# Performance work log

Hardware: AMD Instinct MI355X
Metric: run time of the kernel (lower is better)

## Reference

```python
import math
import jax, jax.numpy as jnp
import numpy as np

B, S, D_MODEL = 2, 4096, 1024
N_HEADS, D_KV = 16, 64
INNER = N_HEADS * D_KV
BLOCK_LEN = 128          # local_radius(127) + 1
GLOBAL_BLOCK = 16
NUM_BUCKETS, MAX_DIST = 32, 128
EPS = 1e-6
NEG = -1e10


def _rel_bucket(rp):
    # T5 bidirectional relative position bucketing
    nb = NUM_BUCKETS // 2
    buckets = jnp.where(rp > 0, nb, 0).astype(jnp.int32)
    rp = jnp.abs(rp)
    max_exact = nb // 2
    is_small = rp < max_exact
    rp_f = jnp.maximum(rp, 1).astype(jnp.float32)
    rp_large = max_exact + (jnp.log(rp_f / max_exact) / math.log(MAX_DIST / max_exact) * (nb - max_exact)).astype(jnp.int32)
    rp_large = jnp.minimum(rp_large, nb - 1)
    return buckets + jnp.where(is_small, rp.astype(jnp.int32), rp_large)


def _concat3(x, block_dim, seq_dim):
    # concatenate [prev, self, next] blocks along seq_dim (zero-padded at edges)
    nblk = x.shape[block_dim]
    pad = [(0, 0)] * x.ndim
    pad[block_dim] = (1, 1)
    xp = jnp.pad(x, pad)
    blocks = [jax.lax.slice_in_dim(xp, i, i + nblk, axis=block_dim) for i in range(3)]
    return jnp.concatenate(blocks, axis=seq_dim)


def _global_block_ids(mask):
    # faithful port of _make_global_fixed_block_ids
    b, s = mask.shape
    fixed = jnp.cumsum(jnp.full_like(mask, 1.0 / GLOBAL_BLOCK), axis=1) - 1.0 / GLOBAL_BLOCK
    m = jnp.where(mask != 0.0, 1.0, -1000.0).astype(mask.dtype)
    gids = jnp.floor(m + fixed - 1.0)
    gids = jnp.maximum(gids, -1.0)
    gids = gids * mask + (mask - 1.0)
    block_ends = (jnp.arange(s) % GLOBAL_BLOCK) == GLOBAL_BLOCK - 1
    true_ends = jnp.logical_and(block_ends[None, :], gids >= 0)
    full_blocks = true_ends.sum(-1, keepdims=True).astype(gids.dtype) - 1.0
    gids = jnp.where(gids < full_blocks, gids, full_blocks)
    ng = s // GLOBAL_BLOCK
    seq_max = jnp.max(gids, axis=-1, keepdims=True)
    gseg = jnp.where(jnp.arange(ng)[None, :] <= seq_max, 1, 0)
    return gids.astype(jnp.int32), gseg.astype(jnp.int32)


def setup_inputs() -> dict:
    key = jax.random.key(0)
    ks = jax.random.split(key, 8)
    sc = D_MODEL ** -0.5
    return {
        "hidden_states": jax.random.normal(ks[0], (B, S, D_MODEL), jnp.float32),
        "mask": jnp.ones((B, S), jnp.float32),
        "Wq": jax.random.normal(ks[1], (D_MODEL, INNER), jnp.float32) * sc,
        "Wk": jax.random.normal(ks[2], (D_MODEL, INNER), jnp.float32) * sc,
        "Wv": jax.random.normal(ks[3], (D_MODEL, INNER), jnp.float32) * sc,
        "Wo": jax.random.normal(ks[4], (INNER, D_MODEL), jnp.float32) * sc,
        "rel_bias": jax.random.normal(ks[5], (NUM_BUCKETS, N_HEADS), jnp.float32),
        "global_rel_bias": jax.random.normal(ks[6], (NUM_BUCKETS, N_HEADS), jnp.float32),
        "ln_weight": jnp.ones((D_MODEL,), jnp.float32),
    }


def reference(hidden_states, mask, Wq, Wk, Wv, Wo, rel_bias, global_rel_bias, ln_weight):
    b, s, _ = hidden_states.shape
    nb = s // BLOCK_LEN

    gids, gseg = _global_block_ids(mask)
    gsl = gseg.shape[-1]  # global_seq_len

    # global aggregates: sum tokens into their fixed global block (pad ids -1 dropped)
    ids = jnp.where(gids >= 0, gids, gsl)
    one_hot = jax.nn.one_hot(ids, gsl + 1, dtype=hidden_states.dtype)[..., :-1]  # (b,s,g)
    global_inputs = jnp.einsum("bnd,bng->bgd", hidden_states, one_hot)
    # LongT5 RMS layernorm (no mean subtraction, no bias)
    var = jnp.mean(global_inputs.astype(jnp.float32) ** 2, axis=-1, keepdims=True)
    global_inputs = ln_weight * (global_inputs * jax.lax.rsqrt(var + EPS))

    heads = lambda x: x.reshape(x.shape[0], x.shape[1], N_HEADS, D_KV)
    q = heads(hidden_states @ Wq).reshape(b, nb, BLOCK_LEN, N_HEADS, D_KV)
    k = heads(hidden_states @ Wk).reshape(b, nb, BLOCK_LEN, N_HEADS, D_KV)
    v = heads(hidden_states @ Wv).reshape(b, nb, BLOCK_LEN, N_HEADS, D_KV)
    side_k = heads(global_inputs @ Wk)  # (b,g,H,dkv)
    side_v = heads(global_inputs @ Wv)

    k3 = _concat3(k, 1, 2)  # (b,nb,3L,H,dkv)
    v3 = _concat3(v, 1, 2)
    side_k = jnp.broadcast_to(side_k[:, None], (b, nb, gsl, N_HEADS, D_KV))
    side_v = jnp.broadcast_to(side_v[:, None], (b, nb, gsl, N_HEADS, D_KV))
    kk = jnp.concatenate([k3, side_k], axis=2)  # (b,nb,3L+g,H,dkv)
    vv = jnp.concatenate([v3, side_v], axis=2)

    # T5-style: no 1/sqrt(d) scaling
    scores = jnp.einsum("bnqhd,bnkhd->bnhqk", q, kk)  # (b,nb,H,L,3L+g)

    # local relative position bias (1,1,H,L,3L)
    mem_pos = jnp.arange(3 * BLOCK_LEN)
    rel_pos = mem_pos[None, :] - mem_pos[BLOCK_LEN:-BLOCK_LEN][:, None]  # (L,3L)
    local_bias = jnp.transpose(rel_bias[_rel_bucket(rel_pos)], (2, 0, 1))[None, None]

    # local attention mask with locality constraint -> (b,nb,1,L,3L)
    bm = mask.reshape(b, nb, BLOCK_LEN)
    bm3 = _concat3(bm, 1, 2)  # (b,nb,3L)
    lam = (bm[..., None] != 0) & (bm3[..., None, :] != 0)  # (b,nb,L,3L)
    lam = lam & (jnp.abs(rel_pos) < BLOCK_LEN)[None, None]
    local_bias = local_bias + jnp.where(lam[:, :, None], 0.0, NEG)  # (b,nb,H,L,3L)

    # side (local->global) bias: mask + relative bias, (b,H,s,g)
    side_mask = mask[:, :, None] == gseg[:, None, :].astype(mask.dtype)
    side_bias = jnp.where(side_mask, 0.0, NEG)[:, None]  # (b,1,s,g)
    side_rel = jnp.arange(gsl)[None, None, :] - gids[:, :, None]  # (b,s,g)
    side_bias = side_bias + jnp.transpose(global_rel_bias[_rel_bucket(side_rel)], (0, 3, 1, 2))
    # -> (b,nb,H,L,g)
    side_bias = side_bias.reshape(b, N_HEADS, nb, BLOCK_LEN, gsl).transpose(0, 2, 1, 3, 4)

    pos_bias = jnp.concatenate([jnp.broadcast_to(local_bias, scores[..., :3 * BLOCK_LEN].shape), side_bias], axis=-1)

    attn = jax.nn.softmax(scores + pos_bias, axis=-1)
    out = jnp.einsum("bnhqk,bnkhd->bnqhd", attn, vv).reshape(b, s, INNER)
    return out[:, :s] @ Wo
```

## Files before the change

### kernel.cpp

```cpp
#include <hip/hip_runtime.h>

typedef _Float16 h16;
typedef __attribute__((ext_vector_type(8))) _Float16 h16x8;
typedef __attribute__((ext_vector_type(4))) float f32x4;

#define G_AS __attribute__((address_space(1)))
#define L_AS __attribute__((address_space(3)))

__device__ __forceinline__ void gload_lds16(const void* g, void* l) {
  __builtin_amdgcn_global_load_lds((G_AS void*)(void*)g, (L_AS void*)l, 16, 0, 0);
}

__device__ __forceinline__ f32x4 mfma16(h16x8 a, h16x8 b, f32x4 c) {
  return __builtin_amdgcn_mfma_f32_16x16x32_f16(a, b, c, 0, 0, 0);
}


__global__ void cvt_f16(const float* __restrict__ in, h16* __restrict__ out, int n) {
  long i = ((long)blockIdx.x * 256 + threadIdx.x) * 8;
  if (i >= n) return;
  float4 a = *(const float4*)(in + i);
  float4 c = *(const float4*)(in + i + 4);
  h16x8 v;
  v[0] = (h16)a.x; v[1] = (h16)a.y; v[2] = (h16)a.z; v[3] = (h16)a.w;
  v[4] = (h16)c.x; v[5] = (h16)c.y; v[6] = (h16)c.z; v[7] = (h16)c.w;
  *(h16x8*)(out + i) = v;
}

__global__ void transpose_cvt(const float* __restrict__ in, h16* __restrict__ out,
                              int rows, int cols) {
  __shared__ float t[32][33];
  int bx = blockIdx.x * 32, by = blockIdx.y * 32;
  int tx = threadIdx.x, ty = threadIdx.y;
#pragma unroll
  for (int j = 0; j < 32; j += 8)
    t[ty + j][tx] = in[(long)(by + ty + j) * cols + bx + tx];
  __syncthreads();
#pragma unroll
  for (int j = 0; j < 32; j += 8)
    out[(long)(bx + ty + j) * rows + by + tx] = (h16)t[tx][ty + j];
}

__global__ __launch_bounds__(256) void global_agg(const float* __restrict__ hs,
                                                  const float* __restrict__ lnw,
                                                  h16* __restrict__ G) {
  const int bg = blockIdx.x;
  const int t = threadIdx.x;
  const float* base = hs + (long)bg * 16384 + t * 4;
  float s0 = 0, s1 = 0, s2 = 0, s3 = 0;
#pragma unroll
  for (int r = 0; r < 16; ++r) {
    float4 x = *(const float4*)(base + r * 1024);
    s0 += x.x; s1 += x.y; s2 += x.z; s3 += x.w;
  }
  float ss = s0 * s0 + s1 * s1 + s2 * s2 + s3 * s3;
#pragma unroll
  for (int msk = 1; msk < 64; msk <<= 1) ss += __shfl_xor(ss, msk);
  __shared__ float red[4];
  if ((t & 63) == 0) red[t >> 6] = ss;
  __syncthreads();
  float tot = red[0] + red[1] + red[2] + red[3];
  float scale = rsqrtf(tot * (1.f / 1024.f) + 1e-6f);
  float4 lw = *(const float4*)(lnw + t * 4);
  h16* o = G + (long)bg * 1024 + t * 4;
  o[0] = (h16)(s0 * scale * lw.x);
  o[1] = (h16)(s1 * scale * lw.y);
  o[2] = (h16)(s2 * scale * lw.z);
  o[3] = (h16)(s3 * scale * lw.w);
}

__device__ __forceinline__ int bucket_of(int rp) {
  int bb = rp > 0 ? 16 : 0;
  int a = rp < 0 ? -rp : rp;
  if (a < 8) return bb + a;
  int n = 31 - __clz(a * a);
  int idx = 8 + (n - 6);
  idx = idx > 15 ? 15 : idx;
  return bb + idx;
}

__global__ void make_tables(const float* __restrict__ rb, const float* __restrict__ grb,
                            float* __restrict__ LT, float* __restrict__ ST) {
  int i = blockIdx.x * 256 + threadIdx.x;
  if (i >= 16 * 511) return;
  int h = i / 511, r = i % 511;
  int rel = r - 255;
  int bkt = bucket_of(rel);
  int a = rel < 0 ? -rel : rel;
  LT[i] = (a <= 127) ? rb[bkt * 16 + h] : -1e10f;
  ST[i] = grb[bkt * 16 + h];
}

template <int OUTF>
__global__ __launch_bounds__(256) void gemm_bt(const h16* __restrict__ A,
                                               const h16* __restrict__ BT,
                                               void* __restrict__ Cout,
                                               int K, int ldc) {
  __shared__ __align__(16) char As[16384];
  __shared__ __align__(16) char Bs[16384];
  const int tid = threadIdx.x;
  const int lane = tid & 63, w = tid >> 6;
  const int l15 = lane & 15, l16 = lane >> 4;
  const long m0 = (long)blockIdx.y * 128;
  const long n0 = (long)blockIdx.x * 128;
  const char* Ab = (const char*)(A + m0 * K);
  const char* Bb = (const char*)(BT + n0 * K);
  const int wr = w >> 1, wc = w & 1;
  const int srow = w * 32 + (lane >> 3);
  const int spk = (lane & 7) * 16;

  f32x4 acc[4][4] = {};
  for (int kt = 0; kt < K; kt += 64) {
#pragma unroll
    for (int i = 0; i < 4; ++i) {
      int row = srow + i * 8;
      int gk = spk ^ ((row & 7) << 4);
      long goff = (long)row * (K * 2) + kt * 2 + gk;
      gload_lds16(Ab + goff, As + (w * 4 + i) * 1024);
      gload_lds16(Bb + goff, Bs + (w * 4 + i) * 1024);
    }
    __syncthreads();
#pragma unroll
    for (int ks = 0; ks < 2; ++ks) {
      h16x8 af[4], bfv[4];
      int kb = ks * 64 + l16 * 16;
#pragma unroll
      for (int i = 0; i < 4; ++i) {
        int ra = wr * 64 + i * 16 + l15;
        af[i] = *(const h16x8*)(As + ra * 128 + (kb ^ ((ra & 7) << 4)));
        int rb2 = wc * 64 + i * 16 + l15;
        bfv[i] = *(const h16x8*)(Bs + rb2 * 128 + (kb ^ ((rb2 & 7) << 4)));
      }
#pragma unroll
      for (int i = 0; i < 4; ++i)
#pragma unroll
        for (int j = 0; j < 4; ++j)
          acc[i][j] = mfma16(af[i], bfv[j], acc[i][j]);
    }
    __syncthreads();
  }
#pragma unroll
  for (int i = 0; i < 4; ++i)
#pragma unroll
    for (int j = 0; j < 4; ++j)
#pragma unroll
      for (int r = 0; r < 4; ++r) {
        long row = m0 + wr * 64 + i * 16 + l16 * 4 + r;
        long col = n0 + wc * 64 + j * 16 + l15;
        if (OUTF == 0)
          ((h16*)Cout)[row * ldc + col] = (h16)acc[i][j][r];
        else
          ((float*)Cout)[row * ldc + col] = acc[i][j][r];
      }
}

__global__ __launch_bounds__(256) void attn_kernel(
    const h16* __restrict__ Qm, const h16* __restrict__ Km,
    const h16* __restrict__ Vt, const h16* __restrict__ SK,
    const h16* __restrict__ SVt, const float* __restrict__ LT,
    const float* __restrict__ ST, h16* __restrict__ AO) {
  __shared__ float lt[512], st[512];
  __shared__ __align__(16) char pbuf[4][4096];
  const int bid = blockIdx.x;
  const int h = bid & 15, blk = (bid >> 4) & 31, b = bid >> 9;
  const int tid = threadIdx.x, lane = tid & 63, w = tid >> 6;
  const int l15 = lane & 15, l16 = lane >> 4;

  for (int i = tid; i < 511; i += 256) {
    lt[i] = LT[h * 511 + i];
    st[i] = ST[h * 511 + i];
  }
  __syncthreads();

  const int qb = blk * 128;
  const long tok0 = (long)b * 4096;

  h16x8 qf[2][2];
#pragma unroll
  for (int i = 0; i < 2; ++i)
#pragma unroll
    for (int ks = 0; ks < 2; ++ks)
      qf[i][ks] = *(const h16x8*)(Qm + (tok0 + qb + w * 32 + i * 16 + l15) * 1024 +
                                  h * 64 + ks * 32 + l16 * 8);

  f32x4 o[2][4] = {};
  float m[2][4], l[2][4];
#pragma unroll
  for (int i = 0; i < 2; ++i)
#pragma unroll
    for (int r = 0; r < 4; ++r) { m[i][r] = -1e30f; l[i][r] = 0.f; }

  char* pb = pbuf[w];

  for (int ci = 0; ci < 10; ++ci) {
    const bool isLocal = ci < 6;
    const int t0 = qb - 128 + ci * 64;
    const int g0 = (ci - 6) * 64;
    if (isLocal && (t0 >= 4096 || t0 < 0)) continue;

    f32x4 s[2][4];
    {
      h16x8 kf[4][2];
#pragma unroll
      for (int j = 0; j < 4; ++j) {
        const h16* kp;
        if (isLocal) {
          int tok = t0 + j * 16 + l15;
          kp = Km + (tok0 + tok) * 1024 + h * 64 + l16 * 8;
        } else {
          int g = g0 + j * 16 + l15;
          kp = SK + ((long)b * 256 + g) * 1024 + h * 64 + l16 * 8;
        }
        kf[j][0] = *(const h16x8*)kp;
        kf[j][1] = *(const h16x8*)(kp + 32);
      }
#pragma unroll
      for (int i = 0; i < 2; ++i)
#pragma unroll
        for (int j = 0; j < 4; ++j) {
          f32x4 t = {};
          t = mfma16(qf[i][0], kf[j][0], t);
          t = mfma16(qf[i][1], kf[j][1], t);
          s[i][j] = t;
        }
    }
#pragma unroll
    for (int i = 0; i < 2; ++i)
#pragma unroll
      for (int r = 0; r < 4; ++r) {
        int tq = qb + w * 32 + i * 16 + l16 * 4 + r;
#pragma unroll
        for (int j = 0; j < 4; ++j) {
          float bias;
          if (isLocal) {
            int tok = t0 + j * 16 + l15;
            bias = lt[tok - tq + 255];
          } else {
            bias = st[g0 + j * 16 + l15 - (tq >> 4) + 255];
          }
          s[i][j][r] += bias;
        }
      }
#pragma unroll
    for (int i = 0; i < 2; ++i)
#pragma unroll
      for (int r = 0; r < 4; ++r) {
        float mx = fmaxf(fmaxf(s[i][0][r], s[i][1][r]), fmaxf(s[i][2][r], s[i][3][r]));
        mx = fmaxf(mx, __shfl_xor(mx, 1));
        mx = fmaxf(mx, __shfl_xor(mx, 2));
        mx = fmaxf(mx, __shfl_xor(mx, 4));
        mx = fmaxf(mx, __shfl_xor(mx, 8));
        float mo = m[i][r];
        float mn = fmaxf(mo, mx);
        float alpha = __expf(mo - mn);
        float rs = 0.f;
#pragma unroll
        for (int j = 0; j < 4; ++j) {
          float p = __expf(s[i][j][r] - mn);
          s[i][j][r] = p;
          rs += p;
        }
        rs += __shfl_xor(rs, 1);
        rs += __shfl_xor(rs, 2);
        rs += __shfl_xor(rs, 4);
        rs += __shfl_xor(rs, 8);
        l[i][r] = l[i][r] * alpha + rs;
        m[i][r] = mn;
#pragma unroll
        for (int df = 0; df < 4; ++df) o[i][df][r] *= alpha;
      }
#pragma unroll
    for (int i = 0; i < 2; ++i)
#pragma unroll
      for (int j = 0; j < 4; ++j)
#pragma unroll
        for (int r = 0; r < 4; ++r) {
          int qi = i * 16 + l16 * 4 + r;
          int byte = qi * 128 + (j * 16 + l15) * 2;
          *(h16*)(pb + (byte ^ ((qi & 7) << 4))) = (h16)s[i][j][r];
        }
#pragma unroll
    for (int ks = 0; ks < 2; ++ks) {
      h16x8 pa[2];
#pragma unroll
      for (int i = 0; i < 2; ++i) {
        int qi = i * 16 + l15;
        int kb = ks * 64 + l16 * 16;
        pa[i] = *(const h16x8*)(pb + qi * 128 + (kb ^ ((qi & 7) << 4)));
      }
      h16x8 vf[4];
#pragma unroll
      for (int df = 0; df < 4; ++df) {
        long vrow = h * 64 + df * 16 + l15;
        if (isLocal) {
          vf[df] = *(const h16x8*)(Vt + vrow * 8192 + tok0 + t0 + ks * 32 + l16 * 8);
        } else {
          vf[df] = *(const h16x8*)(SVt + vrow * 512 + b * 256 + g0 + ks * 32 + l16 * 8);
        }
      }
#pragma unroll
      for (int i = 0; i < 2; ++i)
#pragma unroll
        for (int df = 0; df < 4; ++df)
          o[i][df] = mfma16(pa[i], vf[df], o[i][df]);
    }
  }
#pragma unroll
  for (int i = 0; i < 2; ++i)
#pragma unroll
    for (int r = 0; r < 4; ++r) {
      float inv = 1.f / l[i][r];
      long row = tok0 + qb + w * 32 + i * 16 + l16 * 4 + r;
#pragma unroll
      for (int df = 0; df < 4; ++df)
        AO[row * 1024 + h * 64 + df * 16 + l15] = (h16)(o[i][df][r] * inv);
    }
}

extern "C" void kernel_launch(void* const* d_in, const int* in_sizes, int n_in,
                              void* d_out, int out_size, void* d_ws, size_t ws_size,
                              hipStream_t stream) {
  const float* hs = (const float*)d_in[0];
  const float* Wq = (const float*)d_in[2];
  const float* Wk = (const float*)d_in[3];
  const float* Wv = (const float*)d_in[4];
  const float* Wo = (const float*)d_in[5];
  const float* rb = (const float*)d_in[6];
  const float* grb = (const float*)d_in[7];
  const float* lnw = (const float*)d_in[8];

  char* p = (char*)d_ws;
  auto take = [&](size_t bytes) {
    char* r = p;
    p += (bytes + 255) & ~(size_t)255;
    return r;
  };
  h16* Xb  = (h16*)take(8192l * 1024 * 2);
  h16* WqT = (h16*)take(1024l * 1024 * 2);
  h16* WkT = (h16*)take(1024l * 1024 * 2);
  h16* WvT = (h16*)take(1024l * 1024 * 2);
  h16* WoT = (h16*)take(1024l * 1024 * 2);
  h16* G   = (h16*)take(512l * 1024 * 2);
  h16* Qm  = (h16*)take(8192l * 1024 * 2);
  h16* Km  = (h16*)take(8192l * 1024 * 2);
  h16* Vt  = (h16*)take(1024l * 8192 * 2);
  h16* SK  = (h16*)take(512l * 1024 * 2);
  h16* SVt = (h16*)take(1024l * 512 * 2);
  h16* AO  = (h16*)take(8192l * 1024 * 2);
  float* LT = (float*)take(16l * 511 * 4);
  float* ST = (float*)take(16l * 511 * 4);

  cvt_f16<<<4096, 256, 0, stream>>>(hs, Xb, 8192 * 1024);
  transpose_cvt<<<dim3(32, 32), dim3(32, 8), 0, stream>>>(Wq, WqT, 1024, 1024);
  transpose_cvt<<<dim3(32, 32), dim3(32, 8), 0, stream>>>(Wk, WkT, 1024, 1024);
  transpose_cvt<<<dim3(32, 32), dim3(32, 8), 0, stream>>>(Wv, WvT, 1024, 1024);
  transpose_cvt<<<dim3(32, 32), dim3(32, 8), 0, stream>>>(Wo, WoT, 1024, 1024);
  global_agg<<<512, 256, 0, stream>>>(hs, lnw, G);
  make_tables<<<32, 256, 0, stream>>>(rb, grb, LT, ST);

  gemm_bt<0><<<dim3(8, 64), 256, 0, stream>>>(Xb, WqT, Qm, 1024, 1024);
  gemm_bt<0><<<dim3(8, 64), 256, 0, stream>>>(Xb, WkT, Km, 1024, 1024);
  gemm_bt<0><<<dim3(64, 8), 256, 0, stream>>>(WvT, Xb, Vt, 1024, 8192);
  gemm_bt<0><<<dim3(8, 4), 256, 0, stream>>>(G, WkT, SK, 1024, 1024);
  gemm_bt<0><<<dim3(4, 8), 256, 0, stream>>>(WvT, G, SVt, 1024, 512);

  attn_kernel<<<1024, 256, 0, stream>>>(Qm, Km, Vt, SK, SVt, LT, ST, AO);

  gemm_bt<1><<<dim3(8, 64), 256, 0, stream>>>(AO, WoT, d_out, 1024, 1024);
}
```

Measured before the change: 352.1 us.

## Fuse prep kernels, merge QK/global projections, and streamline attention softmax

Fuses the fp16 conversion of hidden states into the global aggregation kernel and batches the four weight transposes into a single launch. Q and K projections become one GEMM against concatenated weights, with the global tokens appended as extra rows, so side keys and values come from the same GEMMs. The attention kernel now computes S transposed, reduces the row max across fewer lanes, and uses exp2. It rescales lazily only when the max grows by more than a threshold and gets row sums from an MFMA against a ones vector. The trade-offs are extra padded work in the GEMMs (8704 rows) and fp16 range risk from the lazy-max threshold.

```diff
diff --git a/kernel.cpp b/kernel.cpp
--- a/kernel.cpp
+++ b/kernel.cpp
@@ -1,6 +1,7 @@
 #include <hip/hip_runtime.h>
 
 typedef _Float16 h16;
+typedef __attribute__((ext_vector_type(4))) _Float16 h16x4;
 typedef __attribute__((ext_vector_type(8))) _Float16 h16x8;
 typedef __attribute__((ext_vector_type(4))) float f32x4;
 
@@ -15,43 +16,22 @@
   return __builtin_amdgcn_mfma_f32_16x16x32_f16(a, b, c, 0, 0, 0);
 }
 
-
-__global__ void cvt_f16(const float* __restrict__ in, h16* __restrict__ out, int n) {
-  long i = ((long)blockIdx.x * 256 + threadIdx.x) * 8;
-  if (i >= n) return;
-  float4 a = *(const float4*)(in + i);
-  float4 c = *(const float4*)(in + i + 4);
-  h16x8 v;
-  v[0] = (h16)a.x; v[1] = (h16)a.y; v[2] = (h16)a.z; v[3] = (h16)a.w;
-  v[4] = (h16)c.x; v[5] = (h16)c.y; v[6] = (h16)c.z; v[7] = (h16)c.w;
-  *(h16x8*)(out + i) = v;
-}
-
-__global__ void transpose_cvt(const float* __restrict__ in, h16* __restrict__ out,
-                              int rows, int cols) {
-  __shared__ float t[32][33];
-  int bx = blockIdx.x * 32, by = blockIdx.y * 32;
-  int tx = threadIdx.x, ty = threadIdx.y;
-#pragma unroll
-  for (int j = 0; j < 32; j += 8)
-    t[ty + j][tx] = in[(long)(by + ty + j) * cols + bx + tx];
-  __syncthreads();
-#pragma unroll
-  for (int j = 0; j < 32; j += 8)
-    out[(long)(bx + ty + j) * rows + by + tx] = (h16)t[tx][ty + j];
-}
-
-__global__ __launch_bounds__(256) void global_agg(const float* __restrict__ hs,
+__global__ __launch_bounds__(256) void fused_prep(const float* __restrict__ hs,
                                                   const float* __restrict__ lnw,
+                                                  h16* __restrict__ Xb,
                                                   h16* __restrict__ G) {
   const int bg = blockIdx.x;
   const int t = threadIdx.x;
   const float* base = hs + (long)bg * 16384 + t * 4;
+  h16* xout = Xb + (long)bg * 16384 + t * 4;
   float s0 = 0, s1 = 0, s2 = 0, s3 = 0;
 #pragma unroll
   for (int r = 0; r < 16; ++r) {
     float4 x = *(const float4*)(base + r * 1024);
     s0 += x.x; s1 += x.y; s2 += x.z; s3 += x.w;
+    h16x4 v;
+    v[0] = (h16)x.x; v[1] = (h16)x.y; v[2] = (h16)x.z; v[3] = (h16)x.w;
+    *(h16x4*)(xout + r * 1024) = v;
   }
   float ss = s0 * s0 + s1 * s1 + s2 * s2 + s3 * s3;
 #pragma unroll
@@ -67,6 +47,24 @@
   o[1] = (h16)(s1 * scale * lw.y);
   o[2] = (h16)(s2 * scale * lw.z);
   o[3] = (h16)(s3 * scale * lw.w);
+}
+
+__global__ void transpose_w4(const float* __restrict__ s0, const float* __restrict__ s1,
+                             const float* __restrict__ s2, const float* __restrict__ s3,
+                             h16* __restrict__ d0, h16* __restrict__ d1,
+                             h16* __restrict__ d2, h16* __restrict__ d3) {
+  const float* src = blockIdx.z == 0 ? s0 : blockIdx.z == 1 ? s1 : blockIdx.z == 2 ? s2 : s3;
+  h16* dst = blockIdx.z == 0 ? d0 : blockIdx.z == 1 ? d1 : blockIdx.z == 2 ? d2 : d3;
+  __shared__ float t[32][33];
+  int bx = blockIdx.x * 32, by = blockIdx.y * 32;
+  int tx = threadIdx.x, ty = threadIdx.y;
+#pragma unroll
+  for (int j = 0; j < 32; j += 8)
+    t[ty + j][tx] = src[(long)(by + ty + j) * 1024 + bx + tx];
+  __syncthreads();
+#pragma unroll
+  for (int j = 0; j < 32; j += 8)
+    dst[(long)(bx + ty + j) * 1024 + by + tx] = (h16)t[tx][ty + j];
 }
 
 __device__ __forceinline__ int bucket_of(int rp) {
@@ -154,17 +152,17 @@
       }
 }
 
-__global__ __launch_bounds__(256) void attn_kernel(
-    const h16* __restrict__ Qm, const h16* __restrict__ Km,
-    const h16* __restrict__ Vt, const h16* __restrict__ SK,
-    const h16* __restrict__ SVt, const float* __restrict__ LT,
-    const float* __restrict__ ST, h16* __restrict__ AO) {
+__global__ __launch_bounds__(256, 4) void attn_kernel(
+    const h16* __restrict__ QKS, const h16* __restrict__ VtX,
+    const float* __restrict__ LT, const float* __restrict__ ST,
+    h16* __restrict__ AO) {
   __shared__ float lt[512], st[512];
   __shared__ __align__(16) char pbuf[4][4096];
   const int bid = blockIdx.x;
   const int h = bid & 15, blk = (bid >> 4) & 31, b = bid >> 9;
   const int tid = threadIdx.x, lane = tid & 63, w = tid >> 6;
   const int l15 = lane & 15, l16 = lane >> 4;
+  const float L2E = 1.44269504f;
 
   for (int i = tid; i < 511; i += 256) {
     lt[i] = LT[h * 511 + i];
@@ -173,6 +171,7 @@
   __syncthreads();
 
   const int qb = blk * 128;
+  const int qw = qb + w * 32;
   const long tok0 = (long)b * 4096;
 
   h16x8 qf[2][2];
@@ -180,141 +179,131 @@
   for (int i = 0; i < 2; ++i)
 #pragma unroll
     for (int ks = 0; ks < 2; ++ks)
-      qf[i][ks] = *(const h16x8*)(Qm + (tok0 + qb + w * 32 + i * 16 + l15) * 1024 +
+      qf[i][ks] = *(const h16x8*)(QKS + (tok0 + qw + i * 16 + l15) * 2048 +
                                   h * 64 + ks * 32 + l16 * 8);
 
   f32x4 o[2][4] = {};
-  float m[2][4], l[2][4];
-#pragma unroll
-  for (int i = 0; i < 2; ++i)
-#pragma unroll
-    for (int r = 0; r < 4; ++r) { m[i][r] = -1e30f; l[i][r] = 0.f; }
-
+  f32x4 lsum[2] = {};
+  float m[2] = {-1e30f, -1e30f};
   char* pb = pbuf[w];
+
+  h16x8 ones;
+#pragma unroll
+  for (int e = 0; e < 8; ++e) ones[e] = (h16)1.f;
 
   for (int ci = 0; ci < 10; ++ci) {
     const bool isLocal = ci < 6;
     const int t0 = qb - 128 + ci * 64;
     const int g0 = (ci - 6) * 64;
-    if (isLocal && (t0 >= 4096 || t0 < 0)) continue;
+    if (isLocal && (t0 < 0 || t0 >= 4096)) continue;
+    const long krow0 = isLocal ? (tok0 + t0) : (long)(8192 + b * 256 + g0);
+    const long vcol0 = isLocal ? (tok0 + t0) : (long)(8192 + b * 256 + g0);
 
     f32x4 s[2][4];
-    {
-      h16x8 kf[4][2];
+#pragma unroll
+    for (int j = 0; j < 4; ++j) {
+      const h16* kp = QKS + (krow0 + j * 16 + l15) * 2048 + 1024 + h * 64 + l16 * 8;
+      h16x8 k0 = *(const h16x8*)kp;
+      h16x8 k1 = *(const h16x8*)(kp + 32);
+#pragma unroll
+      for (int i = 0; i < 2; ++i) {
+        f32x4 z = {};
+        z = mfma16(k0, qf[i][0], z);
+        z = mfma16(k1, qf[i][1], z);
+        s[i][j] = z;
+      }
+    }
+
+    float mx[2];
+#pragma unroll
+    for (int i = 0; i < 2; ++i) {
+      const float* tbl = isLocal ? lt : st;
+      int bbase = isLocal ? (t0 + l16 * 4 - (qw + i * 16 + l15) + 255)
+                          : (g0 + l16 * 4 - ((qw + i * 16 + l15) >> 4) + 255);
+      float mj[4];
 #pragma unroll
       for (int j = 0; j < 4; ++j) {
-        const h16* kp;
-        if (isLocal) {
-          int tok = t0 + j * 16 + l15;
-          kp = Km + (tok0 + tok) * 1024 + h * 64 + l16 * 8;
-        } else {
-          int g = g0 + j * 16 + l15;
-          kp = SK + ((long)b * 256 + g) * 1024 + h * 64 + l16 * 8;
+#pragma unroll
+        for (int r = 0; r < 4; ++r)
+          s[i][j][r] += tbl[bbase + j * 16 + r];
+        mj[j] = fmaxf(fmaxf(s[i][j][0], s[i][j][1]), fmaxf(s[i][j][2], s[i][j][3]));
+      }
+      float mm = fmaxf(fmaxf(mj[0], mj[1]), fmaxf(mj[2], mj[3]));
+      mm = fmaxf(mm, __shfl_xor(mm, 16));
+      mm = fmaxf(mm, __shfl_xor(mm, 32));
+      mx[i] = mm;
+    }
+
+    bool up = (mx[0] > m[0] + 10.f) || (mx[1] > m[1] + 10.f);
+    if (__any(up)) {
+#pragma unroll
+      for (int i = 0; i < 2; ++i) {
+        float mn = mx[i] > m[i] + 10.f ? mx[i] : m[i];
+        float al = __builtin_amdgcn_exp2f((m[i] - mn) * L2E);
+        m[i] = mn;
+#pragma unroll
+        for (int r = 0; r < 4; ++r) {
+          float ar = __shfl(al, l16 * 4 + r);
+          lsum[i][r] *= ar;
+#pragma unroll
+          for (int df = 0; df < 4; ++df) o[i][df][r] *= ar;
         }
-        kf[j][0] = *(const h16x8*)kp;
-        kf[j][1] = *(const h16x8*)(kp + 32);
-      }
-#pragma unroll
-      for (int i = 0; i < 2; ++i)
-#pragma unroll
-        for (int j = 0; j < 4; ++j) {
-          f32x4 t = {};
-          t = mfma16(qf[i][0], kf[j][0], t);
-          t = mfma16(qf[i][1], kf[j][1], t);
-          s[i][j] = t;
-        }
-    }
-#pragma unroll
-    for (int i = 0; i < 2; ++i)
-#pragma unroll
-      for (int r = 0; r < 4; ++r) {
-        int tq = qb + w * 32 + i * 16 + l16 * 4 + r;
-#pragma unroll
-        for (int j = 0; j < 4; ++j) {
-          float bias;
-          if (isLocal) {
-            int tok = t0 + j * 16 + l15;
-            bias = lt[tok - tq + 255];
-          } else {
-            bias = st[g0 + j * 16 + l15 - (tq >> 4) + 255];
-          }
-          s[i][j][r] += bias;
-        }
-      }
-#pragma unroll
-    for (int i = 0; i < 2; ++i)
-#pragma unroll
-      for (int r = 0; r < 4; ++r) {
-        float mx = fmaxf(fmaxf(s[i][0][r], s[i][1][r]), fmaxf(s[i][2][r], s[i][3][r]));
-        mx = fmaxf(mx, __shfl_xor(mx, 1));
-        mx = fmaxf(mx, __shfl_xor(mx, 2));
-        mx = fmaxf(mx, __shfl_xor(mx, 4));
-        mx = fmaxf(mx, __shfl_xor(mx, 8));
-        float mo = m[i][r];
-        float mn = fmaxf(mo, mx);
-        float alpha = __expf(mo - mn);
-        float rs = 0.f;
-#pragma unroll
-        for (int j = 0; j < 4; ++j) {
-          float p = __expf(s[i][j][r] - mn);
-          s[i][j][r] = p;
-          rs += p;
-        }
-        rs += __shfl_xor(rs, 1);
-        rs += __shfl_xor(rs, 2);
-        rs += __shfl_xor(rs, 4);
-        rs += __shfl_xor(rs, 8);
-        l[i][r] = l[i][r] * alpha + rs;
-        m[i][r] = mn;
-#pragma unroll
-        for (int df = 0; df < 4; ++df) o[i][df][r] *= alpha;
-      }
-#pragma unroll
-    for (int i = 0; i < 2; ++i)
-#pragma unroll
-      for (int j = 0; j < 4; ++j)
-#pragma unroll
-        for (int r = 0; r < 4; ++r) {
-          int qi = i * 16 + l16 * 4 + r;
-          int byte = qi * 128 + (j * 16 + l15) * 2;
-          *(h16*)(pb + (byte ^ ((qi & 7) << 4))) = (h16)s[i][j][r];
-        }
+      }
+    }
+
+#pragma unroll
+    for (int i = 0; i < 2; ++i) {
+      float mi = m[i];
+      int q = i * 16 + l15;
+      int x = (q & 7) << 4;
+      int base = q * 128 + ((l16 * 8) ^ (x & 0x10));
+      int xr = x & 0x60;
+#pragma unroll
+      for (int j = 0; j < 4; ++j) {
+        h16x4 ph;
+#pragma unroll
+        for (int r = 0; r < 4; ++r)
+          ph[r] = (h16)__builtin_amdgcn_exp2f((s[i][j][r] - mi) * L2E);
+        *(h16x4*)(pb + base + ((j * 32) ^ xr)) = ph;
+      }
+    }
+
 #pragma unroll
     for (int ks = 0; ks < 2; ++ks) {
       h16x8 pa[2];
 #pragma unroll
       for (int i = 0; i < 2; ++i) {
-        int qi = i * 16 + l15;
-        int kb = ks * 64 + l16 * 16;
-        pa[i] = *(const h16x8*)(pb + qi * 128 + (kb ^ ((qi & 7) << 4)));
+        int q = i * 16 + l15;
+        int x = (q & 7) << 4;
+        int rb2 = q * 128 + ((l16 * 16) ^ (x & 0x30)) + ((ks * 64) ^ (x & 0x40));
+        pa[i] = *(const h16x8*)(pb + rb2);
       }
       h16x8 vf[4];
 #pragma unroll
-      for (int df = 0; df < 4; ++df) {
-        long vrow = h * 64 + df * 16 + l15;
-        if (isLocal) {
-          vf[df] = *(const h16x8*)(Vt + vrow * 8192 + tok0 + t0 + ks * 32 + l16 * 8);
-        } else {
-          vf[df] = *(const h16x8*)(SVt + vrow * 512 + b * 256 + g0 + ks * 32 + l16 * 8);
-        }
-      }
-#pragma unroll
-      for (int i = 0; i < 2; ++i)
+      for (int df = 0; df < 4; ++df)
+        vf[df] = *(const h16x8*)(VtX + (long)(h * 64 + df * 16 + l15) * 8704 +
+                                 vcol0 + ks * 32 + l16 * 8);
+#pragma unroll
+      for (int i = 0; i < 2; ++i) {
+        lsum[i] = mfma16(pa[i], ones, lsum[i]);
 #pragma unroll
         for (int df = 0; df < 4; ++df)
           o[i][df] = mfma16(pa[i], vf[df], o[i][df]);
-    }
-  }
-#pragma unroll
-  for (int i = 0; i < 2; ++i)
+      }
+    }
+  }
+
+#pragma unroll
+  for (int i = 0; i < 2; ++i) {
 #pragma unroll
     for (int r = 0; r < 4; ++r) {
-      float inv = 1.f / l[i][r];
-      long row = tok0 + qb + w * 32 + i * 16 + l16 * 4 + r;
+      float inv = 1.f / lsum[i][r];
+      long row = tok0 + qw + i * 16 + l16 * 4 + r;
 #pragma unroll
       for (int df = 0; df < 4; ++df)
         AO[row * 1024 + h * 64 + df * 16 + l15] = (h16)(o[i][df][r] * inv);
     }
+  }
 }
 
 extern "C" void kernel_launch(void* const* d_in, const int* in_sizes, int n_in,
@@ -335,36 +324,26 @@
     p += (bytes + 255) & ~(size_t)255;
     return r;
   };
-  h16* Xb  = (h16*)take(8192l * 1024 * 2);
-  h16* WqT = (h16*)take(1024l * 1024 * 2);
-  h16* WkT = (h16*)take(1024l * 1024 * 2);
-  h16* WvT = (h16*)take(1024l * 1024 * 2);
-  h16* WoT = (h16*)take(1024l * 1024 * 2);
-  h16* G   = (h16*)take(512l * 1024 * 2);
-  h16* Qm  = (h16*)take(8192l * 1024 * 2);
-  h16* Km  = (h16*)take(8192l * 1024 * 2);
-  h16* Vt  = (h16*)take(1024l * 8192 * 2);
-  h16* SK  = (h16*)take(512l * 1024 * 2);
-  h16* SVt = (h16*)take(1024l * 512 * 2);
-  h16* AO  = (h16*)take(8192l * 1024 * 2);
+  h16* Xb   = (h16*)take(8704l * 1024 * 2);
+  h16* G    = Xb + 8192l * 1024;
+  h16* WqkT = (h16*)take(2048l * 1024 * 2);
+  h16* WvT  = (h16*)take(1024l * 1024 * 2);
+  h16* WoT  = (h16*)take(1024l * 1024 * 2);
+  h16* QKS  = (h16*)take(8704l * 2048 * 2);
+  h16* VtX  = (h16*)take(1024l * 8704 * 2);
+  h16* AO   = (h16*)take(8192l * 1024 * 2);
   float* LT = (float*)take(16l * 511 * 4);
   float* ST = (float*)take(16l * 511 * 4);
 
-  cvt_f16<<<4096, 256, 0, stream>>>(hs, Xb, 8192 * 1024);
-  transpose_cvt<<<dim3(32, 32), dim3(32, 8), 0, stream>>>(Wq, WqT, 1024, 1024);
-  transpose_cvt<<<dim3(32, 32), dim3(32, 8), 0, stream>>>(Wk, WkT, 1024, 1024);
-  transpose_cvt<<<dim3(32, 32), dim3(32, 8), 0, stream>>>(Wv, WvT, 1024, 1024);
-  transpose_cvt<<<dim3(32, 32), dim3(32, 8), 0, stream>>>(Wo, WoT, 1024, 1024);
-  global_agg<<<512, 256, 0, stream>>>(hs, lnw, G);
+  fused_prep<<<512, 256, 0, stream>>>(hs, lnw, Xb, G);
+  transpose_w4<<<dim3(32, 32, 4), dim3(32, 8), 0, stream>>>(
+      Wq, Wk, Wv, Wo, WqkT, WqkT + 1024l * 1024, WvT, WoT);
   make_tables<<<32, 256, 0, stream>>>(rb, grb, LT, ST);
 
-  gemm_bt<0><<<dim3(8, 64), 256, 0, stream>>>(Xb, WqT, Qm, 1024, 1024);
-  gemm_bt<0><<<dim3(8, 64), 256, 0, stream>>>(Xb, WkT, Km, 1024, 1024);
-  gemm_bt<0><<<dim3(64, 8), 256, 0, stream>>>(WvT, Xb, Vt, 1024, 8192);
-  gemm_bt<0><<<dim3(8, 4), 256, 0, stream>>>(G, WkT, SK, 1024, 1024);
-  gemm_bt<0><<<dim3(4, 8), 256, 0, stream>>>(WvT, G, SVt, 1024, 512);
-
-  attn_kernel<<<1024, 256, 0, stream>>>(Qm, Km, Vt, SK, SVt, LT, ST, AO);
+  gemm_bt<0><<<dim3(16, 68), 256, 0, stream>>>(Xb, WqkT, QKS, 1024, 2048);
+  gemm_bt<0><<<dim3(68, 8), 256, 0, stream>>>(WvT, Xb, VtX, 1024, 8704);
+
+  attn_kernel<<<1024, 256, 0, stream>>>(QKS, VtX, LT, ST, AO);
 
   gemm_bt<1><<<dim3(8, 64), 256, 0, stream>>>(AO, WoT, d_out, 1024, 1024);
 }
```

Measured after the change: 290.0 us. -17.6%, faster.
